# Optimization experiments

Hardware: AMD Instinct MI355X
Metric: run time of the kernel (lower is better)

Reference implementation:

```python
import jax, jax.numpy as jnp
import numpy as np

N_NODES = 100000
N_EDGES = 1000000
IN_DIM = 64
HID = 64
N_CLUSTER = 30
REG = 0.01


def glorot(key, shape):
    lim = np.sqrt(6.0 / (shape[0] + shape[1]))
    return jax.random.uniform(key, shape, jnp.float32, -lim, lim)


def setup_inputs() -> dict:
    key = jax.random.key(0)
    k1, k2, k3, k4, k5 = jax.random.split(key, 5)
    x = jax.random.normal(k1, (N_NODES, IN_DIM), jnp.float32)
    edge_index = jax.random.randint(k2, (2, N_EDGES), 0, N_NODES, jnp.int64)
    edge_attr = jax.random.uniform(k3, (N_EDGES,), jnp.float32)
    W1 = glorot(k4, (IN_DIM, HID))
    b1 = jnp.zeros((HID,), jnp.float32)
    W2 = glorot(k5, (HID, N_CLUSTER))
    b2 = jnp.zeros((N_CLUSTER,), jnp.float32)
    return {"x": x, "edge_index": edge_index, "edge_attr": edge_attr,
            "W1": W1, "b1": b1, "W2": W2, "b2": b2}


def gcn_conv(x, W, b, src, dst, w):
    # PyG GCNConv with edge weights: add self-loops (weight 1), symmetric norm.
    h = x @ W  # [N, out]
    deg = jax.ops.segment_sum(w, dst, num_segments=N_NODES) + 1.0  # self-loop
    dinv = jax.lax.rsqrt(deg)
    norm = dinv[src] * w * dinv[dst]  # [E]
    agg = jax.ops.segment_sum(norm[:, None] * h[src], dst, num_segments=N_NODES)
    agg = agg + h / deg[:, None]  # self-loop contribution: norm = 1/deg
    return agg + b


def reference(x, edge_index, edge_attr, W1, b1, W2, b2):
    src, dst = edge_index[0], edge_index[1]
    h = jax.nn.relu(gcn_conv(x, W1, b1, src, dst, edge_attr))
    # dropout p=0 -> identity
    X2 = gcn_conv(h, W2, b2, src, dst, edge_attr)
    FX = jax.nn.softmax(X2, axis=-1)  # [N, C]
    FF = jnp.sum(FX[src] * FX[dst], axis=-1)  # [E]
    NFX = jnp.log(1.0 - FX ** 2)  # [N, C]
    preg = -jnp.sum(jnp.log(1.0001 - jnp.exp(jnp.sum(NFX, axis=0))))
    loss = jnp.mean((FF - edge_attr) ** 2)
    return FX, loss + REG * preg
```

## Files before the change

kernel.cpp:

```cpp
#include <hip/hip_runtime.h>
#include <hip/hip_fp16.h>
#include <math.h>

#define N_NODES 100000
#define N_EDGES 1000000
#define IN_DIM 64
#define HID 64
#define NC 30
#define NCP 32
#define REG_C 0.01f

#define SCAN_TILE 1024
#define SCAN_NT ((N_NODES + SCAN_TILE - 1) / SCAN_TILE)
#define NTILES (N_NODES / 16)
#define DEG_SCALE 16777216.0f

#define HG_GROUPS 1303
#define HG_GRID (HG_GROUPS * 4)

typedef _Float16 half8 __attribute__((ext_vector_type(8)));
typedef float f32x4 __attribute__((ext_vector_type(4)));

__device__ __forceinline__ unsigned char enc_fp8(float v) {
    return (unsigned char)(__builtin_amdgcn_cvt_pk_fp8_f32(v, v, 0, false) & 0xFF);
}
__device__ __forceinline__ float dec_fp8(unsigned char b) {
    return __builtin_amdgcn_cvt_f32_fp8((int)b, 0);
}
__device__ __forceinline__ float dot4_fp8(unsigned a, unsigned b) {
    float s = __builtin_amdgcn_cvt_f32_fp8((int)a, 0) * __builtin_amdgcn_cvt_f32_fp8((int)b, 0);
    s += __builtin_amdgcn_cvt_f32_fp8((int)a, 1) * __builtin_amdgcn_cvt_f32_fp8((int)b, 1);
    s += __builtin_amdgcn_cvt_f32_fp8((int)a, 2) * __builtin_amdgcn_cvt_f32_fp8((int)b, 2);
    s += __builtin_amdgcn_cvt_f32_fp8((int)a, 3) * __builtin_amdgcn_cvt_f32_fp8((int)b, 3);
    return s;
}

__global__ void hist_gemm(const int* __restrict__ dst, const float* __restrict__ w,
                          unsigned long long* __restrict__ packed, int* __restrict__ rank,
                          const float* __restrict__ X, const float* __restrict__ W,
                          unsigned char* __restrict__ H8) {
    const int g = blockIdx.x;
    const int q = g >> 2, r = g & 3;
    if (r != 3) {
        int hb = g - q;
        int e = hb * 256 + threadIdx.x;
        if (e < N_EDGES) {
            int d = dst[e];
            unsigned long long pk = (1ULL << 40) |
                (unsigned long long)__float2uint_rn(w[e] * DEG_SCALE);
            unsigned long long old = atomicAdd(&packed[d], pk);
            rank[e] = (int)(old >> 40);
        }
        return;
    }
    const int lane = threadIdx.x & 63;
    const int wave = threadIdx.x >> 6;
    const int qd = lane >> 4;
    const int l = lane & 15;
    half8 bfrag[2][4];
#pragma unroll
    for (int kb = 0; kb < 2; ++kb)
#pragma unroll
        for (int t = 0; t < 4; ++t)
#pragma unroll
            for (int j = 0; j < 8; ++j)
                bfrag[kb][t][j] = (_Float16)W[(kb * 32 + qd * 8 + j) * 64 + t * 16 + l];

    const int waveStride = HG_GROUPS * 4;
    for (int ntile = q * 4 + wave; ntile < NTILES; ntile += waveStride) {
        const int node0 = ntile * 16;
        const float* arow = X + (size_t)(node0 + l) * 64 + qd * 8;
        half8 af0, af1;
#pragma unroll
        for (int j = 0; j < 8; ++j) {
            af0[j] = (_Float16)arow[j];
            af1[j] = (_Float16)arow[32 + j];
        }
        f32x4 acc[4];
#pragma unroll
        for (int t = 0; t < 4; ++t) acc[t] = (f32x4){0.f, 0.f, 0.f, 0.f};
#pragma unroll
        for (int t = 0; t < 4; ++t) {
            acc[t] = __builtin_amdgcn_mfma_f32_16x16x32_f16(af0, bfrag[0][t], acc[t], 0, 0, 0);
            acc[t] = __builtin_amdgcn_mfma_f32_16x16x32_f16(af1, bfrag[1][t], acc[t], 0, 0, 0);
        }
#pragma unroll
        for (int t = 0; t < 4; ++t)
#pragma unroll
            for (int rr = 0; rr < 4; ++rr)
                H8[(size_t)(node0 + qd * 4 + rr) * 64 + t * 16 + l] = enc_fp8(acc[t][rr]);
    }
}

__global__ void scan_p1_dinv(const unsigned long long* __restrict__ packed,
                             int* __restrict__ blocksum, float* __restrict__ dinv,
                             float* __restrict__ invdeg) {
    __shared__ int s[256];
    int base = blockIdx.x * SCAN_TILE;
    int tid = threadIdx.x;
    int sum = 0;
#pragma unroll
    for (int j = 0; j < 4; ++j) {
        int i = base + tid * 4 + j;
        if (i < N_NODES) {
            unsigned long long p = packed[i];
            sum += (int)(p >> 40);
            float d = (float)(p & 0xFFFFFFFFFFULL) * (1.0f / DEG_SCALE) + 1.0f;
            dinv[i] = rsqrtf(d);
            invdeg[i] = 1.0f / d;
        }
    }
    s[tid] = sum;
    __syncthreads();
    for (int off = 128; off; off >>= 1) {
        if (tid < off) s[tid] += s[tid + off];
        __syncthreads();
    }
    if (tid == 0) blocksum[blockIdx.x] = s[0];
}

__global__ void scan_p2(int* __restrict__ blocksum, int* __restrict__ rowptr) {
    __shared__ int s[128];
    int tid = threadIdx.x;
    s[tid] = (tid < SCAN_NT) ? blocksum[tid] : 0;
    __syncthreads();
    if (tid == 0) {
        int run = 0;
        for (int i = 0; i < SCAN_NT; ++i) { int v = s[i]; s[i] = run; run += v; }
        rowptr[N_NODES] = N_EDGES;
    }
    __syncthreads();
    if (tid < SCAN_NT) blocksum[tid] = s[tid];
}

__global__ void scan_p3(const unsigned long long* __restrict__ packed,
                        const int* __restrict__ blocksum, int* __restrict__ rowptr) {
    __shared__ int s[256];
    int base = blockIdx.x * SCAN_TILE;
    int tid = threadIdx.x;
    int v[4];
    int sum = 0;
#pragma unroll
    for (int j = 0; j < 4; ++j) {
        int i = base + tid * 4 + j;
        v[j] = (i < N_NODES) ? (int)(packed[i] >> 40) : 0;
        sum += v[j];
    }
    s[tid] = sum;
    __syncthreads();
    for (int off = 1; off < 256; off <<= 1) {
        int t = (tid >= off) ? s[tid - off] : 0;
        __syncthreads();
        s[tid] += t;
        __syncthreads();
    }
    int run = blocksum[blockIdx.x] + (tid ? s[tid - 1] : 0);
#pragma unroll
    for (int j = 0; j < 4; ++j) {
        int i = base + tid * 4 + j;
        if (i < N_NODES) rowptr[i] = run;
        run += v[j];
    }
}

__global__ void sort_scatter(const int* __restrict__ src, const int* __restrict__ dst,
                             const float* __restrict__ w, const float* __restrict__ dinv,
                             const int* __restrict__ rowptr, const int* __restrict__ rank,
                             int2* __restrict__ edata2, int2* __restrict__ wd) {
    int e = blockIdx.x * blockDim.x + threadIdx.x;
    if (e < N_EDGES) {
        int s = src[e], d = dst[e];
        float we = w[e];
        float norm = dinv[s] * we * dinv[d];
        int pos = rowptr[d] + rank[e];
        edata2[pos] = make_int2(s, __float_as_int(norm));
        wd[pos] = make_int2(__float_as_int(we), d);
    }
}

__global__ void agg64_fused(const int* __restrict__ rowptr, const int2* __restrict__ edata2,
                            const unsigned char* __restrict__ H8, const float* __restrict__ invdeg,
                            const float* __restrict__ b1, _Float16* __restrict__ h2h) {
    int node = blockIdx.x * 4 + (threadIdx.x >> 6);
    int lane = threadIdx.x & 63;
    if (node >= N_NODES) return;
    int p = rowptr[node], end = rowptr[node + 1];
    float a0 = 0.f, a1 = 0.f, a2 = 0.f, a3 = 0.f;
    float a4 = 0.f, a5 = 0.f, a6 = 0.f, a7 = 0.f;
    for (; p + 7 < end; p += 8) {
        int2 e0 = edata2[p],     e1 = edata2[p + 1], e2 = edata2[p + 2], e3 = edata2[p + 3];
        int2 e4 = edata2[p + 4], e5 = edata2[p + 5], e6 = edata2[p + 6], e7 = edata2[p + 7];
        a0 += __int_as_float(e0.y) * dec_fp8(H8[(size_t)e0.x * 64 + lane]);
        a1 += __int_as_float(e1.y) * dec_fp8(H8[(size_t)e1.x * 64 + lane]);
        a2 += __int_as_float(e2.y) * dec_fp8(H8[(size_t)e2.x * 64 + lane]);
        a3 += __int_as_float(e3.y) * dec_fp8(H8[(size_t)e3.x * 64 + lane]);
        a4 += __int_as_float(e4.y) * dec_fp8(H8[(size_t)e4.x * 64 + lane]);
        a5 += __int_as_float(e5.y) * dec_fp8(H8[(size_t)e5.x * 64 + lane]);
        a6 += __int_as_float(e6.y) * dec_fp8(H8[(size_t)e6.x * 64 + lane]);
        a7 += __int_as_float(e7.y) * dec_fp8(H8[(size_t)e7.x * 64 + lane]);
    }
    for (; p + 1 < end; p += 2) {
        int2 e0 = edata2[p], e1 = edata2[p + 1];
        a0 += __int_as_float(e0.y) * dec_fp8(H8[(size_t)e0.x * 64 + lane]);
        a1 += __int_as_float(e1.y) * dec_fp8(H8[(size_t)e1.x * 64 + lane]);
    }
    if (p < end) {
        int2 e0 = edata2[p];
        a0 += __int_as_float(e0.y) * dec_fp8(H8[(size_t)e0.x * 64 + lane]);
    }
    float v = ((a0 + a1) + (a2 + a3)) + ((a4 + a5) + (a6 + a7)) +
              dec_fp8(H8[(size_t)node * 64 + lane]) * invdeg[node] + b1[lane];
    h2h[(size_t)node * 64 + lane] = (_Float16)fmaxf(v, 0.f);
}

__global__ void linear30(const _Float16* __restrict__ H, const float* __restrict__ W2,
                         __half* __restrict__ HH16) {
    __shared__ float sW[64 * NC];
    __shared__ float sH[8 * 64];
    for (int i = threadIdx.x; i < 64 * NC; i += blockDim.x) sW[i] = W2[i];
    int node0 = blockIdx.x * 8;
    for (int i = threadIdx.x; i < 8 * 64; i += blockDim.x) {
        int n = node0 + (i >> 6);
        sH[i] = (n < N_NODES) ? (float)H[(size_t)n * 64 + (i & 63)] : 0.f;
    }
    __syncthreads();
    int ln = threadIdx.x >> 5;
    int c = threadIdx.x & 31;
    int node = node0 + ln;
    if (node < N_NODES) {
        float acc = 0.f;
        if (c < NC) {
#pragma unroll
            for (int k = 0; k < 64; ++k) acc += sH[ln * 64 + k] * sW[k * NC + c];
        }
        HH16[(size_t)node * NCP + c] = __float2half(acc);
    }
}

__global__ void agg30_softmax_colsum(const int* __restrict__ rowptr, const int2* __restrict__ edata2,
                                     const __half* __restrict__ HH16,
                                     const float* __restrict__ invdeg,
                                     const float* __restrict__ b2, float* __restrict__ FX,
                                     unsigned char* __restrict__ FX8,
                                     float* __restrict__ colsum_part) {
    const int lane = threadIdx.x & 63;
    const int waveInBlock = threadIdx.x >> 6;
    const int half = lane >> 5;
    const int c = lane & 31;
    const bool activeC = (c < NC);
    const int wavesTotal = gridDim.x * (blockDim.x >> 6);
    const int w0 = blockIdx.x * (blockDim.x >> 6) + waveInBlock;

    const float bb = activeC ? b2[c] : 0.f;
    float lacc = 0.f;

    for (int pair = w0; pair < N_NODES / 2; pair += wavesTotal) {
        const int node = pair * 2 + half;
        int p = rowptr[node], end = rowptr[node + 1];
        float acc0 = 0.f, acc1 = 0.f, acc2 = 0.f, acc3 = 0.f;
        for (; p + 3 < end; p += 4) {
            int2 e0 = edata2[p],     e1 = edata2[p + 1];
            int2 e2 = edata2[p + 2], e3 = edata2[p + 3];
            acc0 += __int_as_float(e0.y) * __half2float(HH16[(size_t)e0.x * NCP + c]);
            acc1 += __int_as_float(e1.y) * __half2float(HH16[(size_t)e1.x * NCP + c]);
            acc2 += __int_as_float(e2.y) * __half2float(HH16[(size_t)e2.x * NCP + c]);
            acc3 += __int_as_float(e3.y) * __half2float(HH16[(size_t)e3.x * NCP + c]);
        }
        for (; p < end; ++p) {
            int2 e0 = edata2[p];
            acc0 += __int_as_float(e0.y) * __half2float(HH16[(size_t)e0.x * NCP + c]);
        }
        float selfv = __half2float(HH16[(size_t)node * NCP + c]);
        float x = activeC ? ((acc0 + acc1) + (acc2 + acc3) + selfv * invdeg[node] + bb)
                          : -INFINITY;
        float mx = x;
        for (int off = 16; off; off >>= 1) mx = fmaxf(mx, __shfl_xor(mx, off));
        float e = activeC ? expf(x - mx) : 0.f;
        float s = e;
        for (int off = 16; off; off >>= 1) s += __shfl_xor(s, off);
        float fx = e / s;
        if (activeC) {
            FX[(size_t)node * NC + c] = fx;
            FX8[(size_t)node * NCP + c] = enc_fp8(fx);
            lacc += log1pf(-fx * fx);
        } else {
            FX8[(size_t)node * NCP + c] = 0;
        }
    }
    lacc += __shfl_xor(lacc, 32);
    __shared__ float part[4][NC];
    if (half == 0 && activeC) part[waveInBlock][c] = lacc;
    __syncthreads();
    if (threadIdx.x < NC) {
        float v = part[0][threadIdx.x] + part[1][threadIdx.x] +
                  part[2][threadIdx.x] + part[3][threadIdx.x];
        atomicAdd(&colsum_part[(blockIdx.x & 63) * 32 + threadIdx.x], v);
    }
}

__global__ void edge_loss_sorted(const int2* __restrict__ edata2, const int2* __restrict__ wd,
                                 const unsigned char* __restrict__ FX8,
                                 float* __restrict__ mse_part) {
    int e = blockIdx.x * blockDim.x + threadIdx.x;
    float v = 0.f;
    if (e < N_EDGES) {
        int2 sn = edata2[e];
        int2 wdv = wd[e];
        const uint4* rs = (const uint4*)(FX8 + (size_t)sn.x * NCP);
        const uint4* rd = (const uint4*)(FX8 + (size_t)wdv.y * NCP);
        uint4 a0 = rs[0], a1 = rs[1];
        uint4 b0 = rd[0], b1 = rd[1];
        float ff = dot4_fp8(a0.x, b0.x) + dot4_fp8(a0.y, b0.y) +
                   dot4_fp8(a0.z, b0.z) + dot4_fp8(a0.w, b0.w) +
                   dot4_fp8(a1.x, b1.x) + dot4_fp8(a1.y, b1.y) +
                   dot4_fp8(a1.z, b1.z) + dot4_fp8(a1.w, b1.w);
        float diff = ff - __int_as_float(wdv.x);
        v = diff * diff;
    }
    for (int off = 32; off > 0; off >>= 1) v += __shfl_down(v, off);
    __shared__ float ps[4];
    int lane = threadIdx.x & 63, wv = threadIdx.x >> 6;
    if (lane == 0) ps[wv] = v;
    __syncthreads();
    if (threadIdx.x == 0)
        atomicAdd(&mse_part[blockIdx.x & 63], ps[0] + ps[1] + ps[2] + ps[3]);
}

__global__ void finalize(const float* __restrict__ colsum_part, const float* __restrict__ mse_part,
                         float* __restrict__ out_loss) {
    int t = threadIdx.x;
    float m = mse_part[t];
    for (int off = 32; off > 0; off >>= 1) m += __shfl_down(m, off);
    float term = 0.f;
    if (t < NC) {
        float s = 0.f;
        for (int k = 0; k < 64; ++k) s += colsum_part[k * 32 + t];
        term = logf(1.0001f - expf(s));
    }
    for (int off = 32; off > 0; off >>= 1) term += __shfl_down(term, off);
    if (t == 0)
        out_loss[0] = m / (float)N_EDGES - REG_C * term;
}

extern "C" void kernel_launch(void* const* d_in, const int* in_sizes, int n_in,
                              void* d_out, int out_size, void* d_ws, size_t ws_size,
                              hipStream_t stream) {
    const float* x  = (const float*)d_in[0];
    const int*   ei = (const int*)d_in[1];
    const float* ea = (const float*)d_in[2];
    const float* W1 = (const float*)d_in[3];
    const float* b1 = (const float*)d_in[4];
    const float* W2 = (const float*)d_in[5];
    const float* b2 = (const float*)d_in[6];
    const int* srcI = ei;
    const int* dstI = ei + N_EDGES;

    float* FX   = (float*)d_out;
    float* loss = FX + (size_t)N_NODES * NC;

    float* ws = (float*)d_ws;
    float*         dinv   = ws;
    float*         invdeg = ws + 100000;
    unsigned char* h8     = (unsigned char*)(ws + 200000);
    _Float16*      h2h    = (_Float16*)(ws + 1800000);
    __half*        hh16   = (__half*)(ws + 5000000);
    unsigned char* fx8    = (unsigned char*)(ws + 6600000);
    float*         colsum_part = ws + 7400000;
    float*         mse_part    = ws + 7402048;
    int*           rowptr = (int*)(ws + 7402112);
    int*           bsum   = (int*)(ws + 7502114);
    unsigned long long* packed = (unsigned long long*)(ws + 7502244);
    int*           rank   = (int*)(ws + 7702244);
    int2*          edata2 = (int2*)(ws + 8702244);
    int2*          wd     = (int2*)(ws + 10702244);

    hipMemsetAsync(packed, 0, N_NODES * sizeof(unsigned long long), stream);
    hipMemsetAsync(colsum_part, 0, (2048 + 64) * sizeof(float), stream);

    hist_gemm<<<HG_GRID, 256, 0, stream>>>(dstI, ea, packed, rank, x, W1, h8);
    scan_p1_dinv<<<SCAN_NT, 256, 0, stream>>>(packed, bsum, dinv, invdeg);
    scan_p2<<<1, 128, 0, stream>>>(bsum, rowptr);
    scan_p3<<<SCAN_NT, 256, 0, stream>>>(packed, bsum, rowptr);
    sort_scatter<<<(N_EDGES + 255) / 256, 256, 0, stream>>>(srcI, dstI, ea, dinv,
                                                            rowptr, rank, edata2, wd);
    agg64_fused<<<(N_NODES + 3) / 4, 256, 0, stream>>>(rowptr, edata2, h8, invdeg, b1, h2h);
    linear30<<<(N_NODES + 7) / 8, 256, 0, stream>>>(h2h, W2, hh16);
    agg30_softmax_colsum<<<4096, 256, 0, stream>>>(rowptr, edata2, hh16, invdeg, b2,
                                                   FX, fx8, colsum_part);
    edge_loss_sorted<<<(N_EDGES + 255) / 256, 256, 0, stream>>>(edata2, wd, fx8, mse_part);
    finalize<<<1, 64, 0, stream>>>(colsum_part, mse_part, loss);
}
```

Before: 318.2 us.

## Replace global-atomic counting sort with two-level bucketed sort using shared-memory atomics

Replaces the per-edge 64-bit global atomic histogram on destination nodes with a two-pass radix-style sort. Edges are first binned into 256-node buckets using block-local shared-memory histograms, a transposed scan and a coarse scatter. Each bucket is then processed by one block that computes degrees, the row pointers and the final CSR scatter with shared-memory atomics. This removes contended global atomics and the packed-degree buffer and memset, at the cost of extra kernel launches and an intermediate pass over the edges. Degree sums now use float atomics, so their order is nondeterministic, and the GEMM grid is resized.

```diff
diff --git a/kernel.cpp b/kernel.cpp
--- a/kernel.cpp
+++ b/kernel.cpp
@@ -10,13 +10,11 @@
 #define NCP 32
 #define REG_C 0.01f
 
-#define SCAN_TILE 1024
-#define SCAN_NT ((N_NODES + SCAN_TILE - 1) / SCAN_TILE)
 #define NTILES (N_NODES / 16)
-#define DEG_SCALE 16777216.0f
-
-#define HG_GROUPS 1303
-#define HG_GRID (HG_GROUPS * 4)
+#define NBUCK 391
+#define EPB_A 2048
+#define NBLK_A 489
+#define GEMM_BLOCKS 512
 
 typedef _Float16 half8 __attribute__((ext_vector_type(8)));
 typedef float f32x4 __attribute__((ext_vector_type(4)));
@@ -35,22 +33,22 @@
     return s;
 }
 
-__global__ void hist_gemm(const int* __restrict__ dst, const float* __restrict__ w,
-                          unsigned long long* __restrict__ packed, int* __restrict__ rank,
+__global__ void hist_gemm(const int* __restrict__ dst, int* __restrict__ histT,
                           const float* __restrict__ X, const float* __restrict__ W,
                           unsigned char* __restrict__ H8) {
-    const int g = blockIdx.x;
-    const int q = g >> 2, r = g & 3;
-    if (r != 3) {
-        int hb = g - q;
-        int e = hb * 256 + threadIdx.x;
-        if (e < N_EDGES) {
-            int d = dst[e];
-            unsigned long long pk = (1ULL << 40) |
-                (unsigned long long)__float2uint_rn(w[e] * DEG_SCALE);
-            unsigned long long old = atomicAdd(&packed[d], pk);
-            rank[e] = (int)(old >> 40);
-        }
+    if (blockIdx.x < NBLK_A) {
+        __shared__ int cnt[NBUCK];
+        for (int i = threadIdx.x; i < NBUCK; i += 256) cnt[i] = 0;
+        __syncthreads();
+        int e0 = blockIdx.x * EPB_A;
+#pragma unroll
+        for (int j = 0; j < 8; ++j) {
+            int e = e0 + j * 256 + threadIdx.x;
+            if (e < N_EDGES) atomicAdd(&cnt[dst[e] >> 8], 1);
+        }
+        __syncthreads();
+        for (int b = threadIdx.x; b < NBUCK; b += 256)
+            histT[b * NBLK_A + blockIdx.x] = cnt[b];
         return;
     }
     const int lane = threadIdx.x & 63;
@@ -66,8 +64,9 @@
             for (int j = 0; j < 8; ++j)
                 bfrag[kb][t][j] = (_Float16)W[(kb * 32 + qd * 8 + j) * 64 + t * 16 + l];
 
-    const int waveStride = HG_GROUPS * 4;
-    for (int ntile = q * 4 + wave; ntile < NTILES; ntile += waveStride) {
+    const int gb = blockIdx.x - NBLK_A;
+    const int waveStride = GEMM_BLOCKS * 4;
+    for (int ntile = gb * 4 + wave; ntile < NTILES; ntile += waveStride) {
         const int node0 = ntile * 16;
         const float* arow = X + (size_t)(node0 + l) * 64 + qd * 8;
         half8 af0, af1;
@@ -92,89 +91,108 @@
     }
 }
 
-__global__ void scan_p1_dinv(const unsigned long long* __restrict__ packed,
-                             int* __restrict__ blocksum, float* __restrict__ dinv,
-                             float* __restrict__ invdeg) {
-    __shared__ int s[256];
-    int base = blockIdx.x * SCAN_TILE;
-    int tid = threadIdx.x;
-    int sum = 0;
-#pragma unroll
-    for (int j = 0; j < 4; ++j) {
-        int i = base + tid * 4 + j;
-        if (i < N_NODES) {
-            unsigned long long p = packed[i];
-            sum += (int)(p >> 40);
-            float d = (float)(p & 0xFFFFFFFFFFULL) * (1.0f / DEG_SCALE) + 1.0f;
-            dinv[i] = rsqrtf(d);
-            invdeg[i] = 1.0f / d;
-        }
-    }
-    s[tid] = sum;
-    __syncthreads();
-    for (int off = 128; off; off >>= 1) {
-        if (tid < off) s[tid] += s[tid + off];
+__global__ void scanA(int* __restrict__ histT, int* __restrict__ bucketTotal) {
+    __shared__ int s[NBLK_A];
+    int b = blockIdx.x;
+    for (int i = threadIdx.x; i < NBLK_A; i += 256) s[i] = histT[b * NBLK_A + i];
+    __syncthreads();
+    if (threadIdx.x == 0) {
+        int run = 0;
+        for (int i = 0; i < NBLK_A; ++i) { int t = s[i]; s[i] = run; run += t; }
+        bucketTotal[b] = run;
+    }
+    __syncthreads();
+    for (int i = threadIdx.x; i < NBLK_A; i += 256) histT[b * NBLK_A + i] = s[i];
+}
+
+__global__ void scanB(const int* __restrict__ bucketTotal, int* __restrict__ bucketBase) {
+    __shared__ int s[NBUCK];
+    for (int i = threadIdx.x; i < NBUCK; i += 256) s[i] = bucketTotal[i];
+    __syncthreads();
+    if (threadIdx.x == 0) {
+        int run = 0;
+        for (int i = 0; i < NBUCK; ++i) { int t = s[i]; s[i] = run; run += t; }
+    }
+    __syncthreads();
+    for (int i = threadIdx.x; i < NBUCK; i += 256) bucketBase[i] = s[i];
+    if (threadIdx.x == 0) bucketBase[NBUCK] = N_EDGES;
+}
+
+__global__ void scatter_coarse(const int* __restrict__ src, const int* __restrict__ dst,
+                               const float* __restrict__ w, const int* __restrict__ histT,
+                               const int* __restrict__ bucketBase,
+                               int2* __restrict__ sw, unsigned char* __restrict__ dl) {
+    __shared__ int cur[NBUCK];
+    int bl = blockIdx.x;
+    for (int b = threadIdx.x; b < NBUCK; b += 256)
+        cur[b] = bucketBase[b] + histT[b * NBLK_A + bl];
+    __syncthreads();
+    int e0 = bl * EPB_A;
+#pragma unroll
+    for (int j = 0; j < 8; ++j) {
+        int e = e0 + j * 256 + threadIdx.x;
+        if (e < N_EDGES) {
+            int d = dst[e];
+            int pos = atomicAdd(&cur[d >> 8], 1);
+            sw[pos] = make_int2(src[e], __float_as_int(w[e]));
+            dl[pos] = (unsigned char)(d & 255);
+        }
+    }
+}
+
+__global__ void bucket_deg(const int2* __restrict__ sw, const unsigned char* __restrict__ dl,
+                           const int* __restrict__ bucketBase, float* __restrict__ dinv,
+                           float* __restrict__ invdeg, int* __restrict__ rowptr) {
+    __shared__ int cnt[256];
+    __shared__ float degf[256];
+    __shared__ int sc[256];
+    int b = blockIdx.x, tid = threadIdx.x;
+    cnt[tid] = 0; degf[tid] = 0.f;
+    __syncthreads();
+    int p0 = bucketBase[b], p1 = bucketBase[b + 1];
+    for (int p = p0 + tid; p < p1; p += 256) {
+        int d = dl[p];
+        atomicAdd(&cnt[d], 1);
+        atomicAdd(&degf[d], __int_as_float(sw[p].y));
+    }
+    __syncthreads();
+    sc[tid] = cnt[tid];
+    __syncthreads();
+    for (int off = 1; off < 256; off <<= 1) {
+        int t = (tid >= off) ? sc[tid - off] : 0;
         __syncthreads();
-    }
-    if (tid == 0) blocksum[blockIdx.x] = s[0];
-}
-
-__global__ void scan_p2(int* __restrict__ blocksum, int* __restrict__ rowptr) {
-    __shared__ int s[128];
-    int tid = threadIdx.x;
-    s[tid] = (tid < SCAN_NT) ? blocksum[tid] : 0;
-    __syncthreads();
-    if (tid == 0) {
-        int run = 0;
-        for (int i = 0; i < SCAN_NT; ++i) { int v = s[i]; s[i] = run; run += v; }
-        rowptr[N_NODES] = N_EDGES;
-    }
-    __syncthreads();
-    if (tid < SCAN_NT) blocksum[tid] = s[tid];
-}
-
-__global__ void scan_p3(const unsigned long long* __restrict__ packed,
-                        const int* __restrict__ blocksum, int* __restrict__ rowptr) {
-    __shared__ int s[256];
-    int base = blockIdx.x * SCAN_TILE;
-    int tid = threadIdx.x;
-    int v[4];
-    int sum = 0;
-#pragma unroll
-    for (int j = 0; j < 4; ++j) {
-        int i = base + tid * 4 + j;
-        v[j] = (i < N_NODES) ? (int)(packed[i] >> 40) : 0;
-        sum += v[j];
-    }
-    s[tid] = sum;
-    __syncthreads();
-    for (int off = 1; off < 256; off <<= 1) {
-        int t = (tid >= off) ? s[tid - off] : 0;
+        sc[tid] += t;
         __syncthreads();
-        s[tid] += t;
-        __syncthreads();
-    }
-    int run = blocksum[blockIdx.x] + (tid ? s[tid - 1] : 0);
-#pragma unroll
-    for (int j = 0; j < 4; ++j) {
-        int i = base + tid * 4 + j;
-        if (i < N_NODES) rowptr[i] = run;
-        run += v[j];
-    }
-}
-
-__global__ void sort_scatter(const int* __restrict__ src, const int* __restrict__ dst,
-                             const float* __restrict__ w, const float* __restrict__ dinv,
-                             const int* __restrict__ rowptr, const int* __restrict__ rank,
-                             int2* __restrict__ edata2, int2* __restrict__ wd) {
-    int e = blockIdx.x * blockDim.x + threadIdx.x;
-    if (e < N_EDGES) {
-        int s = src[e], d = dst[e];
-        float we = w[e];
-        float norm = dinv[s] * we * dinv[d];
-        int pos = rowptr[d] + rank[e];
-        edata2[pos] = make_int2(s, __float_as_int(norm));
-        wd[pos] = make_int2(__float_as_int(we), d);
+    }
+    int node = b * 256 + tid;
+    if (node < N_NODES) {
+        float d = degf[tid] + 1.0f;
+        dinv[node] = rsqrtf(d);
+        invdeg[node] = 1.0f / d;
+        rowptr[node] = p0 + sc[tid] - cnt[tid];
+    }
+    if (b == 0 && tid == 0) rowptr[N_NODES] = N_EDGES;
+}
+
+__global__ void bucket_scatter(const int2* __restrict__ sw, const unsigned char* __restrict__ dl,
+                               const int* __restrict__ bucketBase, const int* __restrict__ rowptr,
+                               const float* __restrict__ dinv,
+                               int2* __restrict__ edata2, int2* __restrict__ wd) {
+    __shared__ int cur[256];
+    __shared__ float ldinv[256];
+    int b = blockIdx.x, tid = threadIdx.x;
+    int node = b * 256 + tid;
+    if (node < N_NODES) { cur[tid] = rowptr[node]; ldinv[tid] = dinv[node]; }
+    __syncthreads();
+    int p0 = bucketBase[b], p1 = bucketBase[b + 1];
+    for (int p = p0 + tid; p < p1; p += 256) {
+        int d = dl[p];
+        int2 r = sw[p];
+        float wv = __int_as_float(r.y);
+        float norm = dinv[r.x] * wv * ldinv[d];
+        int pos = atomicAdd(&cur[d], 1);
+        edata2[pos] = make_int2(r.x, __float_as_int(norm));
+        wd[pos] = make_int2(r.y, b * 256 + d);
     }
 }
 
@@ -368,21 +386,22 @@
     float*         colsum_part = ws + 7400000;
     float*         mse_part    = ws + 7402048;
     int*           rowptr = (int*)(ws + 7402112);
-    int*           bsum   = (int*)(ws + 7502114);
-    unsigned long long* packed = (unsigned long long*)(ws + 7502244);
-    int*           rank   = (int*)(ws + 7702244);
-    int2*          edata2 = (int2*)(ws + 8702244);
-    int2*          wd     = (int2*)(ws + 10702244);
-
-    hipMemsetAsync(packed, 0, N_NODES * sizeof(unsigned long long), stream);
+    int*           histT  = (int*)(ws + 7502114);
+    int*           bucketTotal = (int*)(ws + 7693314);
+    int*           bucketBase  = (int*)(ws + 7693706);
+    int2*          sw     = (int2*)(ws + 7694098);
+    unsigned char* dl     = (unsigned char*)(ws + 9694098);
+    int2*          edata2 = (int2*)(ws + 9944098);
+    int2*          wd     = (int2*)(ws + 11944098);
+
     hipMemsetAsync(colsum_part, 0, (2048 + 64) * sizeof(float), stream);
 
-    hist_gemm<<<HG_GRID, 256, 0, stream>>>(dstI, ea, packed, rank, x, W1, h8);
-    scan_p1_dinv<<<SCAN_NT, 256, 0, stream>>>(packed, bsum, dinv, invdeg);
-    scan_p2<<<1, 128, 0, stream>>>(bsum, rowptr);
-    scan_p3<<<SCAN_NT, 256, 0, stream>>>(packed, bsum, rowptr);
-    sort_scatter<<<(N_EDGES + 255) / 256, 256, 0, stream>>>(srcI, dstI, ea, dinv,
-                                                            rowptr, rank, edata2, wd);
+    hist_gemm<<<NBLK_A + GEMM_BLOCKS, 256, 0, stream>>>(dstI, histT, x, W1, h8);
+    scanA<<<NBUCK, 256, 0, stream>>>(histT, bucketTotal);
+    scanB<<<1, 256, 0, stream>>>(bucketTotal, bucketBase);
+    scatter_coarse<<<NBLK_A, 256, 0, stream>>>(srcI, dstI, ea, histT, bucketBase, sw, dl);
+    bucket_deg<<<NBUCK, 256, 0, stream>>>(sw, dl, bucketBase, dinv, invdeg, rowptr);
+    bucket_scatter<<<NBUCK, 256, 0, stream>>>(sw, dl, bucketBase, rowptr, dinv, edata2, wd);
     agg64_fused<<<(N_NODES + 3) / 4, 256, 0, stream>>>(rowptr, edata2, h8, invdeg, b1, h2h);
     linear30<<<(N_NODES + 7) / 8, 256, 0, stream>>>(h2h, W2, hh16);
     agg30_softmax_colsum<<<4096, 256, 0, stream>>>(rowptr, edata2, hh16, invdeg, b2,
```

After: 303.0 us. 1.05x faster.
